# Kernel tuning notes

Measured on AMD Instinct MI355X. Metric: run time of the kernel, lower is better.

## Reference

```python
import jax, jax.numpy as jnp
import numpy as np

K_TOP = 8
TEMP = 1.0
GUMBEL_EPS = 1e-20
GEN_EPS = 1e-7
NEG_INF = -1e9


def _genconv(xn, src, dst, e, We, be, W1, b1, W2, b2):
    """GENConv: edge-proj, m=relu(x_src+e)+eps, per-dst softmax aggregation (t=1),
    residual add, then 2-layer MLP."""
    N = xn.shape[0]
    ep = e @ We + be                         # [E, C]
    m = jax.nn.relu(xn[src] + ep) + GEN_EPS  # [E, C]
    mx = jax.ops.segment_max(m, dst, num_segments=N)
    mx = jnp.where(jnp.isfinite(mx), mx, 0.0)
    w = jnp.exp(m - mx[dst])
    den = jax.ops.segment_sum(w, dst, num_segments=N)
    agg = jax.ops.segment_sum(w * m, dst, num_segments=N) / jnp.where(den > 0, den, 1.0)
    out = agg + xn
    return jax.nn.relu(out @ W1 + b1) @ W2 + b2


def setup_inputs() -> dict:
    key = jax.random.key(0)
    ks = jax.random.split(key, 16)
    N, E, D, ED = 1024, 16384, 128, 16
    H1, H2, OUT = 64, 64, 40
    s = 0.02
    return {
        "x": jax.random.normal(ks[0], (N, D), jnp.float32),
        "edge_attr": jax.random.normal(ks[1], (E, ED), jnp.float32),
        "gumbel_u": jax.random.uniform(ks[2], (N, N), jnp.float32),
        "mlp_w": jax.random.normal(ks[3], (ED + 2 * D, 1), jnp.float32) * s,
        "mlp_b": jnp.zeros((1,), jnp.float32),
        "c1_we": jax.random.normal(ks[4], (ED, D), jnp.float32) * s,
        "c1_be": jnp.zeros((D,), jnp.float32),
        "c1_w1": jax.random.normal(ks[5], (D, 2 * D), jnp.float32) * s,
        "c1_b1": jnp.zeros((2 * D,), jnp.float32),
        "c1_w2": jax.random.normal(ks[6], (2 * D, H1), jnp.float32) * s,
        "c1_b2": jnp.zeros((H1,), jnp.float32),
        "c2_we": jax.random.normal(ks[7], (ED, H1), jnp.float32) * s,
        "c2_be": jnp.zeros((H1,), jnp.float32),
        "c2_w1": jax.random.normal(ks[8], (H1, 2 * H1), jnp.float32) * s,
        "c2_b1": jnp.zeros((2 * H1,), jnp.float32),
        "c2_w2": jax.random.normal(ks[9], (2 * H1, H2), jnp.float32) * s,
        "c2_b2": jnp.zeros((H2,), jnp.float32),
        "fc_w": jax.random.normal(ks[10], (H2, OUT), jnp.float32) * s,
        "fc_b": jnp.zeros((OUT,), jnp.float32),
        "num_nodes": N,
        "edge_index": jax.random.randint(ks[11], (2, E), 0, N),
        "node_mask": jnp.ones((N,), jnp.int32),
    }


def reference(x, edge_attr, gumbel_u, mlp_w, mlp_b,
              c1_we, c1_be, c1_w1, c1_b1, c1_w2, c1_b2,
              c2_we, c2_be, c2_w1, c2_b1, c2_w2, c2_b2,
              fc_w, fc_b, num_nodes, edge_index, node_mask):
    N, D = x.shape
    src, dst = edge_index[0], edge_index[1]

    # dense adjacency (duplicate edges sum, only used as a zero/nonzero mask)
    adj = jnp.zeros((N, N), x.dtype).at[src, dst].add(1.0)

    # Edge-score MLP on concat([x_u, x_v*mask, edge_attr_dense]) decomposed
    # linearly (same math as scoring the dense [N,N,2D+ED] feature tensor).
    w_node, w_nb, w_e = mlp_w[:D], mlp_w[D:2 * D], mlp_w[2 * D:]
    s_edge = jnp.zeros((N, N), x.dtype).at[src, dst].set((edge_attr @ w_e)[:, 0])
    score = (x @ w_node) + (x @ w_nb).T * (adj > 0) + s_edge + mlp_b[0]
    score = jnp.where(adj == 0, NEG_INF, score)

    z = jax.nn.softmax(score, axis=-1)
    g = -jnp.log(-jnp.log(gumbel_u + GUMBEL_EPS) + GUMBEL_EPS)
    z = jax.nn.softmax((z + g) / TEMP, axis=-1)

    # top-k edge sampling; softmax output is strictly positive so valid_mask
    # (z>0) is always all-True and shapes stay static at N*k edges.
    _, topi = jax.lax.top_k(z, K_TOP)                       # [N, k]
    new_src = jnp.repeat(jnp.arange(N), K_TOP)
    new_dst = topi.reshape(-1)

    # match each new edge against old edge list (argmax of boolean equality,
    # unmatched edges fall back to index 0 exactly as torch argmax does)
    eq = (edge_index[0][None, :] == new_src[:, None]) & \
         (edge_index[1][None, :] == new_dst[:, None])       # [N*k, E]
    new_attr = edge_attr[jnp.argmax(eq, axis=-1)]

    h = _genconv(x, new_src, new_dst, new_attr, c1_we, c1_be, c1_w1, c1_b1, c1_w2, c1_b2)
    h = jax.nn.relu(h)
    h = _genconv(h, new_src, new_dst, new_attr, c2_we, c2_be, c2_w1, c2_b1, c2_w2, c2_b2)
    h = jax.nn.relu(h)
    out = h @ fc_w + fc_b
    # node_mask is all ones, so x[node_mask != 0] == identity; masked write
    # keeps static shapes under jit.
    return jnp.where((node_mask != 0)[:, None], out, 0.0)
```

## Files before the change

### kernel.cpp

```cpp
#include <hip/hip_runtime.h>
#include <cfloat>

#define NN   1024
#define NE   16384
#define D0   128
#define EDIM 16
#define NH1  64
#define NOUT 40
#define KTOP 8
#define NEGINF (-1000000000.0f)
#define MAXDEG 64
#define PMAX   64

#define OFF_EM  0u
#define OFF_ND  32768u
#define OFF_H   65536u

__device__ __forceinline__ void amx(float& v, int& j, float ov, int oj) {
    if (ov > v || (ov == v && oj < j)) { v = ov; j = oj; }
}

__global__ __launch_bounds__(512) void topk_kernel(
    const float* __restrict__ x, const float* __restrict__ ea,
    const float* __restrict__ u, const float* __restrict__ mlp_w,
    const float* __restrict__ mlp_b, const int* __restrict__ ei,
    int* __restrict__ nd, int* __restrict__ em)
{
    __shared__ int   idmx[NN];
    __shared__ int   idmn[NN];
    __shared__ float sv[NN];
    __shared__ int   plj[PMAX];
    __shared__ int   ple[PMAX];
    __shared__ int   np;
    __shared__ float wred[16];
    __shared__ float candv[64];
    __shared__ int   candj[64];
    const int i = blockIdx.x, t = threadIdx.x;
    const int lane = t & 63, w = t >> 6;
    const int subl = t & 15;
    const int gg = t >> 4;

    float uval[2];
    uval[0] = u[i * NN + w * 128 + lane];
    uval[1] = u[i * NN + w * 128 + 64 + lane];

    #pragma unroll
    for (int q = 0; q < 2; q++) {
        int j = t + q * 512;
        idmx[j] = -1; idmn[j] = 0x7FFFFFFF; sv[j] = NEGINF;
    }
    if (t == 0) np = 0;
    __syncthreads();

    const int4* s4 = (const int4*)ei;
    #pragma unroll
    for (int q = 0; q < 8; q++) {
        int idx4 = t + q * 512;
        int4 sv4 = s4[idx4];
        int e0 = idx4 * 4;
        if (sv4.x == i) { int dj = ei[NE + e0 + 0]; atomicMax(&idmx[dj], e0 + 0); atomicMin(&idmn[dj], e0 + 0); }
        if (sv4.y == i) { int dj = ei[NE + e0 + 1]; atomicMax(&idmx[dj], e0 + 1); atomicMin(&idmn[dj], e0 + 1); }
        if (sv4.z == i) { int dj = ei[NE + e0 + 2]; atomicMax(&idmx[dj], e0 + 2); atomicMin(&idmn[dj], e0 + 2); }
        if (sv4.w == i) { int dj = ei[NE + e0 + 3]; atomicMax(&idmx[dj], e0 + 3); atomicMin(&idmn[dj], e0 + 3); }
    }
    __syncthreads();

    #pragma unroll
    for (int q = 0; q < 2; q++) {
        int j = t + q * 512;
        int e = idmx[j];
        if (e >= 0) {
            int p = atomicAdd(&np, 1);
            if (p < PMAX) { plj[p] = j; ple[p] = e; }
        }
    }
    __syncthreads();

    float part = x[i * D0 + lane] * mlp_w[lane] + x[i * D0 + 64 + lane] * mlp_w[64 + lane];
    for (int s2 = 32; s2; s2 >>= 1) part += __shfl_down(part, s2);
    const float arb = __shfl(part, 0) + mlp_b[0];

    const int npc = min(np, PMAX);
    for (int p = gg; p < npc; p += 32) {
        int j = plj[p], e = ple[p];
        float pp = ea[e * EDIM + subl] * mlp_w[2 * D0 + subl];
        #pragma unroll
        for (int k = 0; k < 8; k++)
            pp += x[j * D0 + subl + k * 16] * mlp_w[D0 + subl + k * 16];
        #pragma unroll
        for (int s2 = 8; s2; s2 >>= 1) pp += __shfl_down(pp, s2, 16);
        if (subl == 0) sv[j] = pp + arb;
    }
    __syncthreads();

    float val[2];
    val[0] = sv[w * 128 + lane];
    val[1] = sv[w * 128 + 64 + lane];
    float lm = fmaxf(val[0], val[1]);
    for (int s2 = 32; s2; s2 >>= 1) lm = fmaxf(lm, __shfl_down(lm, s2));
    if (lane == 0) wred[w] = lm;
    __syncthreads();
    float rowmax = wred[0];
    #pragma unroll
    for (int q = 1; q < 8; q++) rowmax = fmaxf(rowmax, wred[q]);
    const bool noedge = (rowmax == NEGINF);

    float ls = 0.f;
    #pragma unroll
    for (int q = 0; q < 2; q++) {
        float ev = noedge ? 1.0f : ((val[q] == NEGINF) ? 0.0f : expf(val[q] - rowmax));
        val[q] = ev; ls += ev;
    }
    for (int s2 = 32; s2; s2 >>= 1) ls += __shfl_down(ls, s2);
    if (lane == 0) wred[8 + w] = ls;
    __syncthreads();
    float rsum = wred[8];
    #pragma unroll
    for (int q = 1; q < 8; q++) rsum += wred[8 + q];

    #pragma unroll
    for (int q = 0; q < 2; q++) {
        float g = -logf(-logf(uval[q] + 1e-20f) + 1e-20f);
        val[q] = val[q] / rsum + g;
    }

    for (int sel = 0; sel < KTOP; sel++) {
        float bv = -FLT_MAX; int bj = NN;
        amx(bv, bj, val[0], w * 128 + lane);
        amx(bv, bj, val[1], w * 128 + 64 + lane);
        for (int s2 = 32; s2; s2 >>= 1) {
            float ov = __shfl_down(bv, s2); int oj = __shfl_down(bj, s2);
            amx(bv, bj, ov, oj);
        }
        int wj = __shfl(bj, 0);
        if (lane == 0) { candv[w * KTOP + sel] = bv; candj[w * KTOP + sel] = bj; }
        if (w * 128 + lane == wj) val[0] = -FLT_MAX;
        if (w * 128 + 64 + lane == wj) val[1] = -FLT_MAX;
    }
    __syncthreads();

    if (w == 0) {
        float mv = candv[lane];
        int   mj = candj[lane];
        for (int sel = 0; sel < KTOP; sel++) {
            float bv = mv; int bj = mj;
            for (int s2 = 32; s2; s2 >>= 1) {
                float ov = __shfl_down(bv, s2); int oj = __shfl_down(bj, s2);
                amx(bv, bj, ov, oj);
            }
            int wj = __shfl(bj, 0);
            if (lane == 0) {
                int mn = idmn[wj];
                em[i * KTOP + sel] = (mn == 0x7FFFFFFF) ? 0 : mn;
                nd[i * KTOP + sel] = wj;
            }
            if (mj == wj) mv = -FLT_MAX;
        }
    }
}

__global__ __launch_bounds__(256) void genconv1_kernel(
    const float* __restrict__ x, const float* __restrict__ ea,
    const float* __restrict__ we_g, const float* __restrict__ be,
    const float* __restrict__ w1, const float* __restrict__ b1,
    const float* __restrict__ w2, const float* __restrict__ b2,
    const int* __restrict__ nd, const int* __restrict__ em,
    float* __restrict__ h)
{
    __shared__ int   slots[2][MAXDEG];
    __shared__ float eatt[2][MAXDEG * EDIM];
    __shared__ float arow[2][D0];
    __shared__ float t1s[2][2 * D0];
    __shared__ int   cnts[2];
    const int t = threadIdx.x, sub = t >> 7, d = t & 127;
    const int r0 = blockIdx.x * 2;
    const int r = r0 + sub;
    if (t < 2) cnts[t] = 0;
    __syncthreads();

    const int4* nd4 = (const int4*)nd;
    #pragma unroll
    for (int q = 0; q < 8; q++) {
        int idx4 = t + q * 256;
        int4 v = nd4[idx4];
        int n0 = idx4 * 4;
        #pragma unroll
        for (int c = 0; c < 4; c++) {
            int dj = (c == 0) ? v.x : (c == 1) ? v.y : (c == 2) ? v.z : v.w;
            unsigned rr = (unsigned)(dj - r0);
            if (rr < 2u) {
                int p = atomicAdd(&cnts[rr], 1);
                if (p < MAXDEG) slots[rr][p] = n0 + c;
            }
        }
    }
    __syncthreads();
    const int cnt = min(cnts[sub], MAXDEG);
    if (d == 0) {
        for (int p = 1; p < cnt; p++) {
            int v = slots[sub][p]; int q = p - 1;
            while (q >= 0 && slots[sub][q] > v) { slots[sub][q + 1] = slots[sub][q]; q--; }
            slots[sub][q + 1] = v;
        }
    }
    __syncthreads();
    for (int q = d; q < cnt * EDIM; q += 128)
        eatt[sub][q] = ea[em[slots[sub][q >> 4]] * EDIM + (q & 15)];
    __syncthreads();

    float wed[EDIM];
    #pragma unroll
    for (int k = 0; k < EDIM; k++) wed[k] = we_g[k * D0 + d];
    const float bed = be[d];

    float mxv = -FLT_MAX;
    for (int idx = 0; idx < cnt; idx++) {
        int src = slots[sub][idx] >> 3;
        float ep = bed;
        #pragma unroll
        for (int k = 0; k < EDIM; k++) ep += eatt[sub][idx * EDIM + k] * wed[k];
        float m = fmaxf(x[src * D0 + d] + ep, 0.f) + 1e-7f;
        mxv = fmaxf(mxv, m);
    }
    float den = 0.f, num = 0.f;
    for (int idx = 0; idx < cnt; idx++) {
        int src = slots[sub][idx] >> 3;
        float ep = bed;
        #pragma unroll
        for (int k = 0; k < EDIM; k++) ep += eatt[sub][idx * EDIM + k] * wed[k];
        float m = fmaxf(x[src * D0 + d] + ep, 0.f) + 1e-7f;
        float w = expf(m - mxv);
        den += w; num += w * m;
    }
    float agg = cnt ? num / (den > 0.f ? den : 1.f) : 0.f;
    arow[sub][d] = agg + x[r * D0 + d];
    __syncthreads();

    float acc0 = b1[d], acc1 = b1[d + D0];
    for (int k = 0; k < D0; k++) {
        float av = arow[sub][k];
        acc0 += av * w1[k * 2 * D0 + d];
        acc1 += av * w1[k * 2 * D0 + d + D0];
    }
    t1s[sub][d] = fmaxf(acc0, 0.f);
    t1s[sub][d + D0] = fmaxf(acc1, 0.f);
    __syncthreads();
    if (d < NH1) {
        float acc = b2[d];
        for (int k = 0; k < 2 * D0; k++) acc += t1s[sub][k] * w2[k * NH1 + d];
        h[r * NH1 + d] = fmaxf(acc, 0.f);
    }
}

__global__ __launch_bounds__(256) void genconv2_kernel(
    const float* __restrict__ h, const float* __restrict__ ea,
    const float* __restrict__ we_g, const float* __restrict__ be,
    const float* __restrict__ w1, const float* __restrict__ b1,
    const float* __restrict__ w2, const float* __restrict__ b2,
    const float* __restrict__ fcw, const float* __restrict__ fcb,
    const int* __restrict__ nd, const int* __restrict__ em,
    const int* __restrict__ mask, float* __restrict__ out)
{
    __shared__ int   slots[4][MAXDEG];
    __shared__ float eatt[4][MAXDEG * EDIM];
    __shared__ float arow[4][NH1];
    __shared__ float t2s[4][2 * NH1];
    __shared__ float h2s[4][NH1];
    __shared__ int   cnts[4];
    const int t = threadIdx.x, sub = t >> 6, d = t & 63;
    const int r0 = blockIdx.x * 4;
    const int r = r0 + sub;
    if (t < 4) cnts[t] = 0;
    __syncthreads();

    const int4* nd4 = (const int4*)nd;
    #pragma unroll
    for (int q = 0; q < 8; q++) {
        int idx4 = t + q * 256;
        int4 v = nd4[idx4];
        int n0 = idx4 * 4;
        #pragma unroll
        for (int c = 0; c < 4; c++) {
            int dj = (c == 0) ? v.x : (c == 1) ? v.y : (c == 2) ? v.z : v.w;
            unsigned rr = (unsigned)(dj - r0);
            if (rr < 4u) {
                int p = atomicAdd(&cnts[rr], 1);
                if (p < MAXDEG) slots[rr][p] = n0 + c;
            }
        }
    }
    __syncthreads();
    const int cnt = min(cnts[sub], MAXDEG);
    if (d == 0) {
        for (int p = 1; p < cnt; p++) {
            int v = slots[sub][p]; int q = p - 1;
            while (q >= 0 && slots[sub][q] > v) { slots[sub][q + 1] = slots[sub][q]; q--; }
            slots[sub][q + 1] = v;
        }
    }
    __syncthreads();
    for (int q = d; q < cnt * EDIM; q += 64)
        eatt[sub][q] = ea[em[slots[sub][q >> 4]] * EDIM + (q & 15)];
    __syncthreads();

    float wed[EDIM];
    #pragma unroll
    for (int k = 0; k < EDIM; k++) wed[k] = we_g[k * NH1 + d];
    const float bed = be[d];

    float mxv = -FLT_MAX;
    for (int idx = 0; idx < cnt; idx++) {
        int src = slots[sub][idx] >> 3;
        float ep = bed;
        #pragma unroll
        for (int k = 0; k < EDIM; k++) ep += eatt[sub][idx * EDIM + k] * wed[k];
        float m = fmaxf(h[src * NH1 + d] + ep, 0.f) + 1e-7f;
        mxv = fmaxf(mxv, m);
    }
    float den = 0.f, num = 0.f;
    for (int idx = 0; idx < cnt; idx++) {
        int src = slots[sub][idx] >> 3;
        float ep = bed;
        #pragma unroll
        for (int k = 0; k < EDIM; k++) ep += eatt[sub][idx * EDIM + k] * wed[k];
        float m = fmaxf(h[src * NH1 + d] + ep, 0.f) + 1e-7f;
        float w = expf(m - mxv);
        den += w; num += w * m;
    }
    float agg = cnt ? num / (den > 0.f ? den : 1.f) : 0.f;
    arow[sub][d] = agg + h[r * NH1 + d];
    __syncthreads();

    {
        float acc_a = b1[d], acc_b = b1[d + NH1];
        for (int k = 0; k < NH1; k++) {
            float av = arow[sub][k];
            acc_a += av * w1[k * 2 * NH1 + d];
            acc_b += av * w1[k * 2 * NH1 + d + NH1];
        }
        t2s[sub][d] = fmaxf(acc_a, 0.f);
        t2s[sub][d + NH1] = fmaxf(acc_b, 0.f);
    }
    __syncthreads();
    {
        float acc = b2[d];
        for (int k = 0; k < 2 * NH1; k++) acc += t2s[sub][k] * w2[k * NH1 + d];
        h2s[sub][d] = fmaxf(acc, 0.f);
    }
    __syncthreads();
    if (d < NOUT) {
        float acc = fcb[d];
        for (int k = 0; k < NH1; k++) acc += h2s[sub][k] * fcw[k * NOUT + d];
        out[r * NOUT + d] = (mask[r] != 0) ? acc : 0.f;
    }
}

extern "C" void kernel_launch(void* const* d_in, const int* in_sizes, int n_in,
                              void* d_out, int out_size, void* d_ws, size_t ws_size,
                              hipStream_t stream) {
    const float* x      = (const float*)d_in[0];
    const float* ea     = (const float*)d_in[1];
    const float* u      = (const float*)d_in[2];
    const float* mlp_w  = (const float*)d_in[3];
    const float* mlp_b  = (const float*)d_in[4];
    const float* c1_we  = (const float*)d_in[5];
    const float* c1_be  = (const float*)d_in[6];
    const float* c1_w1  = (const float*)d_in[7];
    const float* c1_b1  = (const float*)d_in[8];
    const float* c1_w2  = (const float*)d_in[9];
    const float* c1_b2  = (const float*)d_in[10];
    const float* c2_we  = (const float*)d_in[11];
    const float* c2_be  = (const float*)d_in[12];
    const float* c2_w1  = (const float*)d_in[13];
    const float* c2_b1  = (const float*)d_in[14];
    const float* c2_w2  = (const float*)d_in[15];
    const float* c2_b2  = (const float*)d_in[16];
    const float* fc_w   = (const float*)d_in[17];
    const float* fc_b   = (const float*)d_in[18];
    const int*   ei     = (const int*)d_in[20];
    const int*   mask   = (const int*)d_in[21];

    char* ws = (char*)d_ws;
    int*   em = (int*)(ws + OFF_EM);
    int*   nd = (int*)(ws + OFF_ND);
    float* h  = (float*)(ws + OFF_H);
    float* out = (float*)d_out;

    topk_kernel<<<NN, 512, 0, stream>>>(x, ea, u, mlp_w, mlp_b, ei, nd, em);
    genconv1_kernel<<<NN / 2, 256, 0, stream>>>(x, ea, c1_we, c1_be, c1_w1, c1_b1, c1_w2, c1_b2,
                                                nd, em, h);
    genconv2_kernel<<<NN / 4, 256, 0, stream>>>(h, ea, c2_we, c2_be, c2_w1, c2_b1, c2_w2, c2_b2,
                                                fc_w, fc_b, nd, em, mask, out);
}
```

Before: 159.0 us.

## Process one node per block in GENConv kernels and prefetch inputs in topk

```diff
diff --git a/kernel.cpp b/kernel.cpp
--- a/kernel.cpp
+++ b/kernel.cpp
@@ -24,6 +24,7 @@
     const float* __restrict__ x, const float* __restrict__ ea,
     const float* __restrict__ u, const float* __restrict__ mlp_w,
     const float* __restrict__ mlp_b, const int* __restrict__ ei,
+    const float* __restrict__ c1w1,
     int* __restrict__ nd, int* __restrict__ em)
 {
     __shared__ int   idmx[NN];
@@ -156,6 +157,12 @@
             }
             if (mj == wj) mv = -FLT_MAX;
         }
+    } else {
+        float pf = 0.f;
+        if (t < 192)       pf = x[i * D0 + (t - 64)];
+        else if (t < 448)  pf = ea[i * 256 + (t - 192)];
+        else if (t < 480)  pf = c1w1[i * 32 + (t - 448)];
+        asm volatile("" :: "v"(pf));
     }
 }
 
@@ -167,15 +174,14 @@
     const int* __restrict__ nd, const int* __restrict__ em,
     float* __restrict__ h)
 {
-    __shared__ int   slots[2][MAXDEG];
-    __shared__ float eatt[2][MAXDEG * EDIM];
-    __shared__ float arow[2][D0];
-    __shared__ float t1s[2][2 * D0];
-    __shared__ int   cnts[2];
-    const int t = threadIdx.x, sub = t >> 7, d = t & 127;
-    const int r0 = blockIdx.x * 2;
-    const int r = r0 + sub;
-    if (t < 2) cnts[t] = 0;
+    __shared__ int   slots[MAXDEG];
+    __shared__ float eatt[MAXDEG * EDIM];
+    __shared__ float arow[D0];
+    __shared__ float t1s[2 * D0];
+    __shared__ int   cnt_s;
+    const int t = threadIdx.x;
+    const int r = blockIdx.x;
+    if (t == 0) cnt_s = 0;
     __syncthreads();
 
     const int4* nd4 = (const int4*)nd;
@@ -184,71 +190,66 @@
         int idx4 = t + q * 256;
         int4 v = nd4[idx4];
         int n0 = idx4 * 4;
+        if (v.x == r) { int p = atomicAdd(&cnt_s, 1); if (p < MAXDEG) slots[p] = n0 + 0; }
+        if (v.y == r) { int p = atomicAdd(&cnt_s, 1); if (p < MAXDEG) slots[p] = n0 + 1; }
+        if (v.z == r) { int p = atomicAdd(&cnt_s, 1); if (p < MAXDEG) slots[p] = n0 + 2; }
+        if (v.w == r) { int p = atomicAdd(&cnt_s, 1); if (p < MAXDEG) slots[p] = n0 + 3; }
+    }
+    __syncthreads();
+    const int cnt = min(cnt_s, MAXDEG);
+    if (t == 0) {
+        for (int p = 1; p < cnt; p++) {
+            int v = slots[p]; int q = p - 1;
+            while (q >= 0 && slots[q] > v) { slots[q + 1] = slots[q]; q--; }
+            slots[q + 1] = v;
+        }
+    }
+    __syncthreads();
+    for (int q = t; q < cnt * EDIM; q += 256)
+        eatt[q] = ea[em[slots[q >> 4]] * EDIM + (q & 15)];
+    __syncthreads();
+
+    if (t < D0) {
+        const int d = t;
+        float wed[EDIM];
         #pragma unroll
-        for (int c = 0; c < 4; c++) {
-            int dj = (c == 0) ? v.x : (c == 1) ? v.y : (c == 2) ? v.z : v.w;
-            unsigned rr = (unsigned)(dj - r0);
-            if (rr < 2u) {
-                int p = atomicAdd(&cnts[rr], 1);
-                if (p < MAXDEG) slots[rr][p] = n0 + c;
-            }
-        }
-    }
-    __syncthreads();
-    const int cnt = min(cnts[sub], MAXDEG);
-    if (d == 0) {
-        for (int p = 1; p < cnt; p++) {
-            int v = slots[sub][p]; int q = p - 1;
-            while (q >= 0 && slots[sub][q] > v) { slots[sub][q + 1] = slots[sub][q]; q--; }
-            slots[sub][q + 1] = v;
-        }
-    }
-    __syncthreads();
-    for (int q = d; q < cnt * EDIM; q += 128)
-        eatt[sub][q] = ea[em[slots[sub][q >> 4]] * EDIM + (q & 15)];
-    __syncthreads();
-
-    float wed[EDIM];
-    #pragma unroll
-    for (int k = 0; k < EDIM; k++) wed[k] = we_g[k * D0 + d];
-    const float bed = be[d];
-
-    float mxv = -FLT_MAX;
-    for (int idx = 0; idx < cnt; idx++) {
-        int src = slots[sub][idx] >> 3;
-        float ep = bed;
-        #pragma unroll
-        for (int k = 0; k < EDIM; k++) ep += eatt[sub][idx * EDIM + k] * wed[k];
-        float m = fmaxf(x[src * D0 + d] + ep, 0.f) + 1e-7f;
-        mxv = fmaxf(mxv, m);
-    }
-    float den = 0.f, num = 0.f;
-    for (int idx = 0; idx < cnt; idx++) {
-        int src = slots[sub][idx] >> 3;
-        float ep = bed;
-        #pragma unroll
-        for (int k = 0; k < EDIM; k++) ep += eatt[sub][idx * EDIM + k] * wed[k];
-        float m = fmaxf(x[src * D0 + d] + ep, 0.f) + 1e-7f;
-        float w = expf(m - mxv);
-        den += w; num += w * m;
-    }
-    float agg = cnt ? num / (den > 0.f ? den : 1.f) : 0.f;
-    arow[sub][d] = agg + x[r * D0 + d];
-    __syncthreads();
-
-    float acc0 = b1[d], acc1 = b1[d + D0];
-    for (int k = 0; k < D0; k++) {
-        float av = arow[sub][k];
-        acc0 += av * w1[k * 2 * D0 + d];
-        acc1 += av * w1[k * 2 * D0 + d + D0];
-    }
-    t1s[sub][d] = fmaxf(acc0, 0.f);
-    t1s[sub][d + D0] = fmaxf(acc1, 0.f);
-    __syncthreads();
-    if (d < NH1) {
-        float acc = b2[d];
-        for (int k = 0; k < 2 * D0; k++) acc += t1s[sub][k] * w2[k * NH1 + d];
-        h[r * NH1 + d] = fmaxf(acc, 0.f);
+        for (int k = 0; k < EDIM; k++) wed[k] = we_g[k * D0 + d];
+        const float bed = be[d];
+
+        float mxv = -FLT_MAX;
+        for (int idx = 0; idx < cnt; idx++) {
+            int src = slots[idx] >> 3;
+            float ep = bed;
+            #pragma unroll
+            for (int k = 0; k < EDIM; k++) ep += eatt[idx * EDIM + k] * wed[k];
+            float m = fmaxf(x[src * D0 + d] + ep, 0.f) + 1e-7f;
+            mxv = fmaxf(mxv, m);
+        }
+        float den = 0.f, num = 0.f;
+        for (int idx = 0; idx < cnt; idx++) {
+            int src = slots[idx] >> 3;
+            float ep = bed;
+            #pragma unroll
+            for (int k = 0; k < EDIM; k++) ep += eatt[idx * EDIM + k] * wed[k];
+            float m = fmaxf(x[src * D0 + d] + ep, 0.f) + 1e-7f;
+            float w = expf(m - mxv);
+            den += w; num += w * m;
+        }
+        float agg = cnt ? num / (den > 0.f ? den : 1.f) : 0.f;
+        arow[d] = agg + x[r * D0 + d];
+    }
+    __syncthreads();
+
+    {
+        float acc = b1[t];
+        for (int k = 0; k < D0; k++) acc += arow[k] * w1[k * 2 * D0 + t];
+        t1s[t] = fmaxf(acc, 0.f);
+    }
+    __syncthreads();
+    if (t < NH1) {
+        float acc = b2[t];
+        for (int k = 0; k < 2 * D0; k++) acc += t1s[k] * w2[k * NH1 + t];
+        h[r * NH1 + t] = fmaxf(acc, 0.f);
     }
 }
 
@@ -261,16 +262,15 @@
     const int* __restrict__ nd, const int* __restrict__ em,
     const int* __restrict__ mask, float* __restrict__ out)
 {
-    __shared__ int   slots[4][MAXDEG];
-    __shared__ float eatt[4][MAXDEG * EDIM];
-    __shared__ float arow[4][NH1];
-    __shared__ float t2s[4][2 * NH1];
-    __shared__ float h2s[4][NH1];
-    __shared__ int   cnts[4];
-    const int t = threadIdx.x, sub = t >> 6, d = t & 63;
-    const int r0 = blockIdx.x * 4;
-    const int r = r0 + sub;
-    if (t < 4) cnts[t] = 0;
+    __shared__ int   slots[MAXDEG];
+    __shared__ float eatt[MAXDEG * EDIM];
+    __shared__ float arow[NH1];
+    __shared__ float t2s[2 * NH1];
+    __shared__ float h2s[NH1];
+    __shared__ int   cnt_s;
+    const int t = threadIdx.x;
+    const int r = blockIdx.x;
+    if (t == 0) cnt_s = 0;
     __syncthreads();
 
     const int4* nd4 = (const int4*)nd;
@@ -279,79 +279,72 @@
         int idx4 = t + q * 256;
         int4 v = nd4[idx4];
         int n0 = idx4 * 4;
+        if (v.x == r) { int p = atomicAdd(&cnt_s, 1); if (p < MAXDEG) slots[p] = n0 + 0; }
+        if (v.y == r) { int p = atomicAdd(&cnt_s, 1); if (p < MAXDEG) slots[p] = n0 + 1; }
+        if (v.z == r) { int p = atomicAdd(&cnt_s, 1); if (p < MAXDEG) slots[p] = n0 + 2; }
+        if (v.w == r) { int p = atomicAdd(&cnt_s, 1); if (p < MAXDEG) slots[p] = n0 + 3; }
+    }
+    __syncthreads();
+    const int cnt = min(cnt_s, MAXDEG);
+    if (t == 0) {
+        for (int p = 1; p < cnt; p++) {
+            int v = slots[p]; int q = p - 1;
+            while (q >= 0 && slots[q] > v) { slots[q + 1] = slots[q]; q--; }
+            slots[q + 1] = v;
+        }
+    }
+    __syncthreads();
+    for (int q = t; q < cnt * EDIM; q += 256)
+        eatt[q] = ea[em[slots[q >> 4]] * EDIM + (q & 15)];
+    __syncthreads();
+
+    if (t < NH1) {
+        const int d = t;
+        float wed[EDIM];
         #pragma unroll
-        for (int c = 0; c < 4; c++) {
-            int dj = (c == 0) ? v.x : (c == 1) ? v.y : (c == 2) ? v.z : v.w;
-            unsigned rr = (unsigned)(dj - r0);
-            if (rr < 4u) {
-                int p = atomicAdd(&cnts[rr], 1);
-                if (p < MAXDEG) slots[rr][p] = n0 + c;
-            }
-        }
-    }
-    __syncthreads();
-    const int cnt = min(cnts[sub], MAXDEG);
-    if (d == 0) {
-        for (int p = 1; p < cnt; p++) {
-            int v = slots[sub][p]; int q = p - 1;
-            while (q >= 0 && slots[sub][q] > v) { slots[sub][q + 1] = slots[sub][q]; q--; }
-            slots[sub][q + 1] = v;
-        }
-    }
-    __syncthreads();
-    for (int q = d; q < cnt * EDIM; q += 64)
-        eatt[sub][q] = ea[em[slots[sub][q >> 4]] * EDIM + (q & 15)];
-    __syncthreads();
-
-    float wed[EDIM];
-    #pragma unroll
-    for (int k = 0; k < EDIM; k++) wed[k] = we_g[k * NH1 + d];
-    const float bed = be[d];
-
-    float mxv = -FLT_MAX;
-    for (int idx = 0; idx < cnt; idx++) {
-        int src = slots[sub][idx] >> 3;
-        float ep = bed;
-        #pragma unroll
-        for (int k = 0; k < EDIM; k++) ep += eatt[sub][idx * EDIM + k] * wed[k];
-        float m = fmaxf(h[src * NH1 + d] + ep, 0.f) + 1e-7f;
-        mxv = fmaxf(mxv, m);
-    }
-    float den = 0.f, num = 0.f;
-    for (int idx = 0; idx < cnt; idx++) {
-        int src = slots[sub][idx] >> 3;
-        float ep = bed;
-        #pragma unroll
-        for (int k = 0; k < EDIM; k++) ep += eatt[sub][idx * EDIM + k] * wed[k];
-        float m = fmaxf(h[src * NH1 + d] + ep, 0.f) + 1e-7f;
-        float w = expf(m - mxv);
-        den += w; num += w * m;
-    }
-    float agg = cnt ? num / (den > 0.f ? den : 1.f) : 0.f;
-    arow[sub][d] = agg + h[r * NH1 + d];
-    __syncthreads();
-
-    {
-        float acc_a = b1[d], acc_b = b1[d + NH1];
-        for (int k = 0; k < NH1; k++) {
-            float av = arow[sub][k];
-            acc_a += av * w1[k * 2 * NH1 + d];
-            acc_b += av * w1[k * 2 * NH1 + d + NH1];
-        }
-        t2s[sub][d] = fmaxf(acc_a, 0.f);
-        t2s[sub][d + NH1] = fmaxf(acc_b, 0.f);
-    }
-    __syncthreads();
-    {
-        float acc = b2[d];
-        for (int k = 0; k < 2 * NH1; k++) acc += t2s[sub][k] * w2[k * NH1 + d];
-        h2s[sub][d] = fmaxf(acc, 0.f);
-    }
-    __syncthreads();
-    if (d < NOUT) {
-        float acc = fcb[d];
-        for (int k = 0; k < NH1; k++) acc += h2s[sub][k] * fcw[k * NOUT + d];
-        out[r * NOUT + d] = (mask[r] != 0) ? acc : 0.f;
+        for (int k = 0; k < EDIM; k++) wed[k] = we_g[k * NH1 + d];
+        const float bed = be[d];
+
+        float mxv = -FLT_MAX;
+        for (int idx = 0; idx < cnt; idx++) {
+            int src = slots[idx] >> 3;
+            float ep = bed;
+            #pragma unroll
+            for (int k = 0; k < EDIM; k++) ep += eatt[idx * EDIM + k] * wed[k];
+            float m = fmaxf(h[src * NH1 + d] + ep, 0.f) + 1e-7f;
+            mxv = fmaxf(mxv, m);
+        }
+        float den = 0.f, num = 0.f;
+        for (int idx = 0; idx < cnt; idx++) {
+            int src = slots[idx] >> 3;
+            float ep = bed;
+            #pragma unroll
+            for (int k = 0; k < EDIM; k++) ep += eatt[idx * EDIM + k] * wed[k];
+            float m = fmaxf(h[src * NH1 + d] + ep, 0.f) + 1e-7f;
+            float w = expf(m - mxv);
+            den += w; num += w * m;
+        }
+        float agg = cnt ? num / (den > 0.f ? den : 1.f) : 0.f;
+        arow[d] = agg + h[r * NH1 + d];
+    }
+    __syncthreads();
+
+    if (t < 2 * NH1) {
+        float acc = b1[t];
+        for (int k = 0; k < NH1; k++) acc += arow[k] * w1[k * 2 * NH1 + t];
+        t2s[t] = fmaxf(acc, 0.f);
+    }
+    __syncthreads();
+    if (t < NH1) {
+        float acc = b2[t];
+        for (int k = 0; k < 2 * NH1; k++) acc += t2s[k] * w2[k * NH1 + t];
+        h2s[t] = fmaxf(acc, 0.f);
+    }
+    __syncthreads();
+    if (t < NOUT) {
+        float acc = fcb[t];
+        for (int k = 0; k < NH1; k++) acc += h2s[k] * fcw[k * NOUT + t];
+        out[r * NOUT + t] = (mask[r] != 0) ? acc : 0.f;
     }
 }
 
@@ -386,9 +379,9 @@
     float* h  = (float*)(ws + OFF_H);
     float* out = (float*)d_out;
 
-    topk_kernel<<<NN, 512, 0, stream>>>(x, ea, u, mlp_w, mlp_b, ei, nd, em);
-    genconv1_kernel<<<NN / 2, 256, 0, stream>>>(x, ea, c1_we, c1_be, c1_w1, c1_b1, c1_w2, c1_b2,
-                                                nd, em, h);
-    genconv2_kernel<<<NN / 4, 256, 0, stream>>>(h, ea, c2_we, c2_be, c2_w1, c2_b1, c2_w2, c2_b2,
-                                                fc_w, fc_b, nd, em, mask, out);
-}
+    topk_kernel<<<NN, 512, 0, stream>>>(x, ea, u, mlp_w, mlp_b, ei, c1_w1, nd, em);
+    genconv1_kernel<<<NN, 256, 0, stream>>>(x, ea, c1_we, c1_be, c1_w1, c1_b1, c1_w2, c1_b2,
+                                            nd, em, h);
+    genconv2_kernel<<<NN, 256, 0, stream>>>(h, ea, c2_we, c2_be, c2_w1, c2_b1, c2_w2, c2_b2,
+                                            fc_w, fc_b, nd, em, mask, out);
+}
```

After: 156.4 us. About the same (-1.7%).
